# Performance work log

Hardware: AMD Instinct MI355X
Metric: run time of the kernel (lower is better)

The kernel has to match this reference:

```python
import jax, jax.numpy as jnp
import numpy as np

N_NODES = 50000


def _sage_conv(x, edge_index, W_l, W_r, b):
    """PyG SAGEConv (aggr='mean', root_weight=True):
    out[i] = mean_{j: (j->i) in E} x[j] @ W_l + x[i] @ W_r + b
    """
    src, dst = edge_index[0], edge_index[1]
    msgs = x[src]                                   # [E, d] gather
    agg = jax.ops.segment_sum(msgs, dst, num_segments=N_NODES)  # [N, d]
    deg = jax.ops.segment_sum(jnp.ones_like(dst, dtype=x.dtype), dst,
                              num_segments=N_NODES)
    agg = agg / jnp.maximum(deg, 1.0)[:, None]      # mean aggregation
    return agg @ W_l + x @ W_r + b


def setup_inputs() -> dict:
    key = jax.random.key(0)
    ks = jax.random.split(key, 8)
    d_in, d_hid, d_out = 128, 128, 64
    n_edges = 640000
    x = jax.random.normal(ks[0], (N_NODES, d_in), dtype=jnp.float32)
    edge_index = jax.random.randint(ks[1], (2, n_edges), 0, N_NODES, dtype=jnp.int32)
    s1 = 1.0 / np.sqrt(d_in)
    s2 = 1.0 / np.sqrt(d_hid)
    return {
        "x": x,
        "edge_index": edge_index,
        "W1_l": jax.random.uniform(ks[2], (d_in, d_hid), jnp.float32, -s1, s1),
        "W1_r": jax.random.uniform(ks[3], (d_in, d_hid), jnp.float32, -s1, s1),
        "b1": jnp.zeros((d_hid,), jnp.float32),
        "W2_l": jax.random.uniform(ks[4], (d_hid, d_out), jnp.float32, -s2, s2),
        "W2_r": jax.random.uniform(ks[5], (d_hid, d_out), jnp.float32, -s2, s2),
        "b2": jnp.zeros((d_out,), jnp.float32),
    }


def reference(x, edge_index, W1_l, W1_r, b1, W2_l, W2_r, b2):
    h = _sage_conv(x, edge_index, W1_l, W1_r, b1)
    h = jax.nn.relu(h)
    # Dropout(0.3) is identity in eval mode.
    return _sage_conv(h, edge_index, W2_l, W2_r, b2)
```

## Files before the change

kernel.cpp:

```cpp
#include <hip/hip_runtime.h>
#include <hip/hip_fp16.h>


typedef _Float16 half8 __attribute__((ext_vector_type(8)));
typedef float floatx4 __attribute__((ext_vector_type(4)));

#define NB 256
#define PA 320

__global__ __launch_bounds__(256) void prep_deg_kernel(const float* __restrict__ x,
                                                       const float* __restrict__ W1l, const float* __restrict__ W1r,
                                                       const float* __restrict__ W2l, const float* __restrict__ W2r,
                                                       _Float16* __restrict__ Ah,
                                                       _Float16* __restrict__ Bp1, _Float16* __restrict__ Bp2,
                                                       const int* __restrict__ dst, int* __restrict__ degi,
                                                       int N, int E) {
    int nconv = (N * 64 + 255) / 256;
    int b = blockIdx.x;
    int tid = threadIdx.x;
    if (b < nconv) {
        int i = b * 256 + tid;
        if (i < N * 64) {
            int row = i >> 6, c = i & 63;
            float2 v = ((const float2*)x)[(size_t)row * 64 + c];
            __half2 h2 = __floats2half2_rn(v.x, v.y);
            *(__half2*)(Ah + (size_t)row * 256 + 128 + c * 2) = h2;
        }
    } else if (b < nconv + 128) {
        int t = (b - nconv) * 256 + tid;
        int j = t & 7, lane = (t >> 3) & 63, nrep = (t >> 9) & 7, kt = t >> 12;
        int k = kt * 32 + ((lane >> 4) * 8) + j;
        int col = nrep * 16 + (lane & 15);
        float v = (k < 128) ? W1l[k * 128 + col] : W1r[(k - 128) * 128 + col];
        Bp1[t] = (_Float16)v;
    } else if (b < nconv + 192) {
        int t = (b - nconv - 128) * 256 + tid;
        int j = t & 7, lane = (t >> 3) & 63, nrep = (t >> 9) & 7, kt = t >> 12;
        int k = kt * 32 + ((lane >> 4) * 8) + j;
        int col = nrep * 16 + (lane & 15);
        float v = (col < 64) ? W2l[k * 64 + col] : W2r[k * 64 + (col - 64)];
        Bp2[t] = (_Float16)v;
    } else {
        int i = (b - nconv - 192) * 256 + tid;
        int E4 = E >> 2;
        if (i < E4) {
            int4 d = ((const int4*)dst)[i];
            atomicAdd(&degi[d.x], 1);
            atomicAdd(&degi[d.y], 1);
            atomicAdd(&degi[d.z], 1);
            atomicAdd(&degi[d.w], 1);
        }
        if (i == 0) {
            for (int e = E4 << 2; e < E; ++e) atomicAdd(&degi[dst[e]], 1);
        }
    }
}

__global__ __launch_bounds__(256) void scan_pass1(const int* __restrict__ deg, int* __restrict__ incl,
                                                  int* __restrict__ bsum, int N) {
    int tid = threadIdx.x;
    int i = blockIdx.x * 256 + tid;
    int v = (i < N) ? deg[i] : 0;
    int lane = tid & 63, wid = tid >> 6;
    int s = v;
#pragma unroll
    for (int off = 1; off < 64; off <<= 1) { int t = __shfl_up(s, off); if (lane >= off) s += t; }
    __shared__ int ws[4], wo[4];
    if (lane == 63) ws[wid] = s;
    __syncthreads();
    if (tid == 0) { int a = 0; for (int w = 0; w < 4; ++w) { wo[w] = a; a += ws[w]; } bsum[blockIdx.x] = a; }
    __syncthreads();
    s += wo[wid];
    if (i < N) incl[i] = s;
}

__global__ __launch_bounds__(256) void scan_pass3f(const int* __restrict__ incl, const int* __restrict__ bsum,
                                                   const int* __restrict__ degi,
                                                   int* __restrict__ rp, float* __restrict__ inv,
                                                   int* __restrict__ bcur, int N, int nper, int nblk) {
    __shared__ int sx[256];
    int tid = threadIdx.x;
    int v = (tid < nblk) ? bsum[tid] : 0;
    int lane = tid & 63, wid = tid >> 6;
    int s = v;
#pragma unroll
    for (int off = 1; off < 64; off <<= 1) { int t = __shfl_up(s, off); if (lane >= off) s += t; }
    __shared__ int ws[4], wo[4];
    if (lane == 63) ws[wid] = s;
    __syncthreads();
    if (tid == 0) { int a = 0; for (int w = 0; w < 4; ++w) { wo[w] = a; a += ws[w]; } }
    __syncthreads();
    sx[tid] = s + wo[wid] - v;
    __syncthreads();
    int boffv = sx[blockIdx.x];
    int i = blockIdx.x * 256 + tid;
    if (i < N) {
        int r = boffv + incl[i];
        rp[i + 1] = r;
        inv[i] = 1.0f / fmaxf((float)degi[i], 1.0f);
        if (i == 0) { rp[0] = 0; bcur[0] = 0; }
        int ip1 = i + 1;
        if (ip1 % nper == 0 && ip1 / nper < NB) bcur[ip1 / nper] = r;
    }
}

__global__ __launch_bounds__(256) void partA_kernel(const int* __restrict__ src, const int* __restrict__ dst,
                                                    int* __restrict__ bcur, unsigned int* __restrict__ bek,
                                                    int E, int nper) {
    __shared__ int cnt[NB], base[NB], cur[NB];
    int tid = threadIdx.x;
    int chunk = (E + PA - 1) / PA;
    int e0 = blockIdx.x * chunk;
    int e1 = min(e0 + chunk, E);
    cnt[tid] = 0;
    cur[tid] = 0;
    __syncthreads();
    for (int e = e0 + tid; e < e1; e += 256) {
        int d = dst[e];
        atomicAdd(&cnt[d / nper], 1);
    }
    __syncthreads();
    int c = cnt[tid];
    base[tid] = (c > 0) ? atomicAdd(&bcur[tid], c) : 0;
    __syncthreads();
    for (int e = e0 + tid; e < e1; e += 256) {
        int d = dst[e];
        int b = d / nper;
        int pos = base[b] + atomicAdd(&cur[b], 1);
        bek[pos] = ((unsigned int)src[e] << 8) | (unsigned int)(d - b * nper);
    }
}

__global__ __launch_bounds__(256) void partB_kernel(const unsigned int* __restrict__ bek,
                                                    const int* __restrict__ rp, int* __restrict__ csr,
                                                    int N, int nper) {
    __shared__ int rps[256], cur[256];
    int k = blockIdx.x;
    int lo = k * nper;
    int hi = min(lo + nper, N);
    int cntN = hi - lo;
    if (cntN <= 0) return;
    int tid = threadIdx.x;
    if (tid < cntN) { rps[tid] = rp[lo + tid]; cur[tid] = 0; }
    __syncthreads();
    int ebeg = rp[lo], eend = rp[hi];
    for (int j = ebeg + tid; j < eend; j += 256) {
        unsigned int u = bek[j];
        int loc = (int)(u & 0xffu);
        int s = (int)(u >> 8);
        int pos = rps[loc] + atomicAdd(&cur[loc], 1);
        csr[pos] = s;
    }
}

__global__ __launch_bounds__(256) void agg128h_kernel(const int* __restrict__ rp, const int* __restrict__ ci,
                                                      _Float16* __restrict__ Ah,
                                                      const float* __restrict__ inv, int N) {
    int node = (blockIdx.x * 256 + threadIdx.x) >> 6;
    int lane = threadIdx.x & 63;
    if (node >= N) return;
    int beg = rp[node], end = rp[node + 1];
    const uint* xu = (const uint*)Ah;
    float2 acc = make_float2(0.f, 0.f);
    for (int base = beg; base < end; base += 64) {
        int idx = base + lane;
        int sv = (idx < end) ? ci[idx] : 0;
        int cnt = min(64, end - base);
        int j = 0;
        for (; j + 8 <= cnt; j += 8) {
            uint u[8];
#pragma unroll
            for (int w = 0; w < 8; ++w) {
                int s = __shfl(sv, j + w);
                u[w] = xu[(size_t)s * 128 + 64 + lane];
            }
#pragma unroll
            for (int w = 0; w < 8; ++w) {
                float2 f = __half22float2(*(const __half2*)&u[w]);
                acc.x += f.x; acc.y += f.y;
            }
        }
        for (; j + 4 <= cnt; j += 4) {
            uint u[4];
#pragma unroll
            for (int w = 0; w < 4; ++w) {
                int s = __shfl(sv, j + w);
                u[w] = xu[(size_t)s * 128 + 64 + lane];
            }
#pragma unroll
            for (int w = 0; w < 4; ++w) {
                float2 f = __half22float2(*(const __half2*)&u[w]);
                acc.x += f.x; acc.y += f.y;
            }
        }
        for (; j < cnt; ++j) {
            int s = __shfl(sv, j);
            uint u = xu[(size_t)s * 128 + 64 + lane];
            float2 f = __half22float2(*(const __half2*)&u);
            acc.x += f.x; acc.y += f.y;
        }
    }
    float iv = inv[node];
    __half2 o = __floats2half2_rn(acc.x * iv, acc.y * iv);
    ((uint*)Ah)[(size_t)node * 128 + lane] = *(const uint*)&o;
}

__global__ __launch_bounds__(256) void agg64h_kernel(const int* __restrict__ rp, const int* __restrict__ ci,
                                                     const _Float16* __restrict__ hl,
                                                     const float* __restrict__ inv,
                                                     float* __restrict__ out, int N) {
    int node = (blockIdx.x * 256 + threadIdx.x) >> 5;
    int sl = threadIdx.x & 31;
    if (node >= N) return;
    int beg = rp[node], end = rp[node + 1];
    const uint* hu = (const uint*)hl;
    float2 acc = make_float2(0.f, 0.f);
    for (int base = beg; base < end; base += 32) {
        int idx = base + sl;
        int sv = (idx < end) ? ci[idx] : 0;
        int cnt = min(32, end - base);
        int j = 0;
        for (; j + 8 <= cnt; j += 8) {
            uint u[8];
#pragma unroll
            for (int w = 0; w < 8; ++w) {
                int s = __shfl(sv, j + w, 32);
                u[w] = hu[(size_t)s * 32 + sl];
            }
#pragma unroll
            for (int w = 0; w < 8; ++w) {
                float2 f = __half22float2(*(const __half2*)&u[w]);
                acc.x += f.x; acc.y += f.y;
            }
        }
        for (; j + 4 <= cnt; j += 4) {
            uint u[4];
#pragma unroll
            for (int w = 0; w < 4; ++w) {
                int s = __shfl(sv, j + w, 32);
                u[w] = hu[(size_t)s * 32 + sl];
            }
#pragma unroll
            for (int w = 0; w < 4; ++w) {
                float2 f = __half22float2(*(const __half2*)&u[w]);
                acc.x += f.x; acc.y += f.y;
            }
        }
        for (; j < cnt; ++j) {
            int s = __shfl(sv, j, 32);
            uint u = hu[(size_t)s * 32 + sl];
            float2 f = __half22float2(*(const __half2*)&u);
            acc.x += f.x; acc.y += f.y;
        }
    }
    float iv = inv[node];
    float2* op = (float2*)(out + (size_t)node * 64 + sl * 2);
    float2 cur = *op;
    cur.x += iv * acc.x;
    cur.y += iv * acc.y;
    *op = cur;
}

__global__ __launch_bounds__(256) void gemm1_mfma(const _Float16* __restrict__ Ah,
                                                  const _Float16* __restrict__ Bp,
                                                  const float* __restrict__ b1,
                                                  _Float16* __restrict__ hh, int N) {
    int wid = threadIdx.x >> 6, lane = threadIdx.x & 63;
    int r = lane & 15, q = lane >> 4;
    int rowbase = blockIdx.x * 128 + wid * 32;
    size_t ra = (size_t)min(rowbase + r, N - 1);
    size_t rb = (size_t)min(rowbase + 16 + r, N - 1);
    const half8* B8 = (const half8*)Bp;

    floatx4 acc[2][8];
#pragma unroll
    for (int m = 0; m < 2; ++m)
#pragma unroll
        for (int n = 0; n < 8; ++n) acc[m][n] = (floatx4){0.f, 0.f, 0.f, 0.f};

#pragma unroll
    for (int kt = 0; kt < 8; ++kt) {
        int k0 = kt * 32 + q * 8;
        half8 a0 = *(const half8*)(Ah + ra * 256 + k0);
        half8 a1 = *(const half8*)(Ah + rb * 256 + k0);
#pragma unroll
        for (int n = 0; n < 8; ++n) {
            half8 bf = B8[(kt * 8 + n) * 64 + lane];
            acc[0][n] = __builtin_amdgcn_mfma_f32_16x16x32_f16(a0, bf, acc[0][n], 0, 0, 0);
            acc[1][n] = __builtin_amdgcn_mfma_f32_16x16x32_f16(a1, bf, acc[1][n], 0, 0, 0);
        }
    }
    float bias[8];
#pragma unroll
    for (int n = 0; n < 8; ++n) bias[n] = b1[n * 16 + r];
#pragma unroll
    for (int m = 0; m < 2; ++m)
#pragma unroll
        for (int reg = 0; reg < 4; ++reg) {
            int row = rowbase + m * 16 + q * 4 + reg;
            if (row < N) {
                _Float16* p = hh + (size_t)row * 128 + r;
#pragma unroll
                for (int n = 0; n < 8; ++n)
                    p[n * 16] = (_Float16)fmaxf(acc[m][n][reg] + bias[n], 0.f);
            }
        }
}

__global__ __launch_bounds__(256) void gemm2_mfma(const _Float16* __restrict__ hh,
                                                  const _Float16* __restrict__ Bp,
                                                  const float* __restrict__ b2,
                                                  _Float16* __restrict__ hl,
                                                  float* __restrict__ outp, int N) {
    int wid = threadIdx.x >> 6, lane = threadIdx.x & 63;
    int r = lane & 15, q = lane >> 4;
    int rowbase = blockIdx.x * 128 + wid * 32;
    size_t ra = (size_t)min(rowbase + r, N - 1);
    size_t rb = (size_t)min(rowbase + 16 + r, N - 1);
    const half8* B8 = (const half8*)Bp;

    floatx4 acc[2][8];
#pragma unroll
    for (int m = 0; m < 2; ++m)
#pragma unroll
        for (int n = 0; n < 8; ++n) acc[m][n] = (floatx4){0.f, 0.f, 0.f, 0.f};

#pragma unroll
    for (int kt = 0; kt < 4; ++kt) {
        int k0 = kt * 32 + q * 8;
        half8 a0 = *(const half8*)(hh + ra * 128 + k0);
        half8 a1 = *(const half8*)(hh + rb * 128 + k0);
#pragma unroll
        for (int n = 0; n < 8; ++n) {
            half8 bf = B8[(kt * 8 + n) * 64 + lane];
            acc[0][n] = __builtin_amdgcn_mfma_f32_16x16x32_f16(a0, bf, acc[0][n], 0, 0, 0);
            acc[1][n] = __builtin_amdgcn_mfma_f32_16x16x32_f16(a1, bf, acc[1][n], 0, 0, 0);
        }
    }
    float bias[4];
#pragma unroll
    for (int n = 0; n < 4; ++n) bias[n] = b2[n * 16 + r];
#pragma unroll
    for (int m = 0; m < 2; ++m)
#pragma unroll
        for (int reg = 0; reg < 4; ++reg) {
            int row = rowbase + m * 16 + q * 4 + reg;
            if (row < N) {
                _Float16* ph = hl + (size_t)row * 64 + r;
                float* po = outp + (size_t)row * 64 + r;
#pragma unroll
                for (int n = 0; n < 4; ++n)
                    ph[n * 16] = (_Float16)acc[m][n][reg];
#pragma unroll
                for (int n = 0; n < 4; ++n)
                    po[n * 16] = acc[m][n + 4][reg] + bias[n];
            }
        }
}

extern "C" void kernel_launch(void* const* d_in, const int* in_sizes, int n_in,
                              void* d_out, int out_size, void* d_ws, size_t ws_size,
                              hipStream_t stream) {
    const float* x   = (const float*)d_in[0];
    const int*   ei  = (const int*)d_in[1];
    const float* W1l = (const float*)d_in[2];
    const float* W1r = (const float*)d_in[3];
    const float* b1  = (const float*)d_in[4];
    const float* W2l = (const float*)d_in[5];
    const float* W2r = (const float*)d_in[6];
    const float* b2  = (const float*)d_in[7];
    float* out = (float*)d_out;

    const int N = in_sizes[0] / 128;
    const int E = in_sizes[1] / 2;
    const int* srcv = ei;
    const int* dstv = ei + E;
    const int nper = (N + NB - 1) / NB;

    _Float16* Ah  = (_Float16*)d_ws;
    _Float16* hh  = Ah + (size_t)N * 256;
    _Float16* hl  = hh + (size_t)N * 128;
    _Float16* Bp1 = hl + (size_t)N * 64;
    _Float16* Bp2 = Bp1 + 32768;
    float* inv  = (float*)(Bp2 + 16384);
    int*   rp   = (int*)(inv + N);
    int*   degi = rp + (N + 1);
    int*   incl = degi + N;
    int*   csr  = incl + N;
    unsigned int* bek = (unsigned int*)(csr + E);
    int*   bsum = (int*)(bek + E);
    int*   bcur = bsum + 256;

    const int nsblk = (N + 255) / 256;

    hipMemsetAsync(degi, 0, (size_t)N * sizeof(int), stream);

    int nconv = (N * 64 + 255) / 256;
    int ndeg = ((E >> 2) + 255) / 256;
    prep_deg_kernel<<<nconv + 192 + ndeg, 256, 0, stream>>>(x, W1l, W1r, W2l, W2r,
                                                            Ah, Bp1, Bp2, dstv, degi, N, E);

    scan_pass1<<<nsblk, 256, 0, stream>>>(degi, incl, bsum, N);
    scan_pass3f<<<nsblk, 256, 0, stream>>>(incl, bsum, degi, rp, inv, bcur, N, nper, nsblk);

    partA_kernel<<<PA, 256, 0, stream>>>(srcv, dstv, bcur, bek, E, nper);
    partB_kernel<<<NB, 256, 0, stream>>>(bek, rp, csr, N, nper);

    agg128h_kernel<<<(N * 64 + 255) / 256, 256, 0, stream>>>(rp, csr, Ah, inv, N);
    int nb = (N + 127) / 128;
    gemm1_mfma<<<nb, 256, 0, stream>>>(Ah, Bp1, b1, hh, N);

    gemm2_mfma<<<nb, 256, 0, stream>>>(hh, Bp2, b2, hl, out, N);
    agg64h_kernel<<<(N * 32 + 255) / 256, 256, 0, stream>>>(rp, csr, hl, inv, out, N);
}
```

Baseline: 149.9 us.

## Replace per-node degree scan with bucket histogram and in-bucket local scan

Drops the global per-node degree atomics and the two-pass N-element scan. Prep now builds a 256-bucket histogram in shared memory, a single-block kernel scans it, and partB computes per-node counts, row pointers and inverse degrees locally within each bucket. This removes a memset of N ints, global atomic contention and two kernel launches, at the cost of an extra pass over bucketed edges in partB.

```diff
diff --git a/kernel.cpp b/kernel.cpp
--- a/kernel.cpp
+++ b/kernel.cpp
@@ -7,14 +7,16 @@
 
 #define NB 256
 #define PA 320
-
-__global__ __launch_bounds__(256) void prep_deg_kernel(const float* __restrict__ x,
-                                                       const float* __restrict__ W1l, const float* __restrict__ W1r,
-                                                       const float* __restrict__ W2l, const float* __restrict__ W2r,
-                                                       _Float16* __restrict__ Ah,
-                                                       _Float16* __restrict__ Bp1, _Float16* __restrict__ Bp2,
-                                                       const int* __restrict__ dst, int* __restrict__ degi,
-                                                       int N, int E) {
+#define HB 320
+
+__global__ __launch_bounds__(256) void prep_hist_kernel(const float* __restrict__ x,
+                                                        const float* __restrict__ W1l, const float* __restrict__ W1r,
+                                                        const float* __restrict__ W2l, const float* __restrict__ W2r,
+                                                        _Float16* __restrict__ Ah,
+                                                        _Float16* __restrict__ Bp1, _Float16* __restrict__ Bp2,
+                                                        const int* __restrict__ dst, int* __restrict__ ghist,
+                                                        int N, int E, int nper) {
+    __shared__ int lh[NB];
     int nconv = (N * 64 + 255) / 256;
     int b = blockIdx.x;
     int tid = threadIdx.x;
@@ -41,26 +43,22 @@
         float v = (col < 64) ? W2l[k * 64 + col] : W2r[k * 64 + (col - 64)];
         Bp2[t] = (_Float16)v;
     } else {
-        int i = (b - nconv - 192) * 256 + tid;
-        int E4 = E >> 2;
-        if (i < E4) {
-            int4 d = ((const int4*)dst)[i];
-            atomicAdd(&degi[d.x], 1);
-            atomicAdd(&degi[d.y], 1);
-            atomicAdd(&degi[d.z], 1);
-            atomicAdd(&degi[d.w], 1);
-        }
-        if (i == 0) {
-            for (int e = E4 << 2; e < E; ++e) atomicAdd(&degi[dst[e]], 1);
-        }
-    }
-}
-
-__global__ __launch_bounds__(256) void scan_pass1(const int* __restrict__ deg, int* __restrict__ incl,
-                                                  int* __restrict__ bsum, int N) {
+        int hb = b - nconv - 192;
+        lh[tid] = 0;
+        __syncthreads();
+        int chunk = (E + HB - 1) / HB;
+        int e0 = hb * chunk, e1 = min(e0 + chunk, E);
+        for (int e = e0 + tid; e < e1; e += 256) atomicAdd(&lh[dst[e] / nper], 1);
+        __syncthreads();
+        int c = lh[tid];
+        if (c) atomicAdd(&ghist[tid], c);
+    }
+}
+
+__global__ __launch_bounds__(256) void scan256_kernel(const int* __restrict__ ghist,
+                                                      int* __restrict__ bbase, int* __restrict__ bcur) {
     int tid = threadIdx.x;
-    int i = blockIdx.x * 256 + tid;
-    int v = (i < N) ? deg[i] : 0;
+    int v = ghist[tid];
     int lane = tid & 63, wid = tid >> 6;
     int s = v;
 #pragma unroll
@@ -68,40 +66,12 @@
     __shared__ int ws[4], wo[4];
     if (lane == 63) ws[wid] = s;
     __syncthreads();
-    if (tid == 0) { int a = 0; for (int w = 0; w < 4; ++w) { wo[w] = a; a += ws[w]; } bsum[blockIdx.x] = a; }
+    if (tid == 0) { int a = 0; for (int w = 0; w < 4; ++w) { wo[w] = a; a += ws[w]; } }
     __syncthreads();
     s += wo[wid];
-    if (i < N) incl[i] = s;
-}
-
-__global__ __launch_bounds__(256) void scan_pass3f(const int* __restrict__ incl, const int* __restrict__ bsum,
-                                                   const int* __restrict__ degi,
-                                                   int* __restrict__ rp, float* __restrict__ inv,
-                                                   int* __restrict__ bcur, int N, int nper, int nblk) {
-    __shared__ int sx[256];
-    int tid = threadIdx.x;
-    int v = (tid < nblk) ? bsum[tid] : 0;
-    int lane = tid & 63, wid = tid >> 6;
-    int s = v;
-#pragma unroll
-    for (int off = 1; off < 64; off <<= 1) { int t = __shfl_up(s, off); if (lane >= off) s += t; }
-    __shared__ int ws[4], wo[4];
-    if (lane == 63) ws[wid] = s;
-    __syncthreads();
-    if (tid == 0) { int a = 0; for (int w = 0; w < 4; ++w) { wo[w] = a; a += ws[w]; } }
-    __syncthreads();
-    sx[tid] = s + wo[wid] - v;
-    __syncthreads();
-    int boffv = sx[blockIdx.x];
-    int i = blockIdx.x * 256 + tid;
-    if (i < N) {
-        int r = boffv + incl[i];
-        rp[i + 1] = r;
-        inv[i] = 1.0f / fmaxf((float)degi[i], 1.0f);
-        if (i == 0) { rp[0] = 0; bcur[0] = 0; }
-        int ip1 = i + 1;
-        if (ip1 % nper == 0 && ip1 / nper < NB) bcur[ip1 / nper] = r;
-    }
+    bbase[tid] = s - v;
+    bcur[tid]  = s - v;
+    if (tid == 255) bbase[NB] = s;
 }
 
 __global__ __launch_bounds__(256) void partA_kernel(const int* __restrict__ src, const int* __restrict__ dst,
@@ -131,25 +101,45 @@
     }
 }
 
-__global__ __launch_bounds__(256) void partB_kernel(const unsigned int* __restrict__ bek,
-                                                    const int* __restrict__ rp, int* __restrict__ csr,
-                                                    int N, int nper) {
-    __shared__ int rps[256], cur[256];
+__global__ __launch_bounds__(256) void partB2_kernel(const unsigned int* __restrict__ bek,
+                                                     const int* __restrict__ bbase,
+                                                     int* __restrict__ rp, float* __restrict__ inv,
+                                                     int* __restrict__ csr, int N, int nper) {
+    __shared__ int lcnt[256], excl[256], cur[256];
+    __shared__ int ws[4], wo[4];
     int k = blockIdx.x;
     int lo = k * nper;
     int hi = min(lo + nper, N);
     int cntN = hi - lo;
     if (cntN <= 0) return;
     int tid = threadIdx.x;
-    if (tid < cntN) { rps[tid] = rp[lo + tid]; cur[tid] = 0; }
-    __syncthreads();
-    int ebeg = rp[lo], eend = rp[hi];
+    lcnt[tid] = 0; cur[tid] = 0;
+    __syncthreads();
+    int ebeg = bbase[k], eend = bbase[k + 1];
+    for (int j = ebeg + tid; j < eend; j += 256)
+        atomicAdd(&lcnt[bek[j] & 0xffu], 1);
+    __syncthreads();
+    int v = lcnt[tid];
+    int lane = tid & 63, wid = tid >> 6;
+    int s = v;
+#pragma unroll
+    for (int off = 1; off < 64; off <<= 1) { int t = __shfl_up(s, off); if (lane >= off) s += t; }
+    if (lane == 63) ws[wid] = s;
+    __syncthreads();
+    if (tid == 0) { int a = 0; for (int w = 0; w < 4; ++w) { wo[w] = a; a += ws[w]; } }
+    __syncthreads();
+    excl[tid] = s + wo[wid] - v;
+    __syncthreads();
+    if (tid <= cntN) {
+        int node = lo + tid;
+        if (node <= N) rp[node] = ebeg + excl[tid];
+        if (tid < cntN) inv[node] = 1.0f / fmaxf((float)lcnt[tid], 1.0f);
+    }
     for (int j = ebeg + tid; j < eend; j += 256) {
         unsigned int u = bek[j];
         int loc = (int)(u & 0xffu);
-        int s = (int)(u >> 8);
-        int pos = rps[loc] + atomicAdd(&cur[loc], 1);
-        csr[pos] = s;
+        int pos = ebeg + excl[loc] + atomicAdd(&cur[loc], 1);
+        csr[pos] = (int)(u >> 8);
     }
 }
 
@@ -384,27 +374,21 @@
     _Float16* Bp2 = Bp1 + 32768;
     float* inv  = (float*)(Bp2 + 16384);
     int*   rp   = (int*)(inv + N);
-    int*   degi = rp + (N + 1);
-    int*   incl = degi + N;
-    int*   csr  = incl + N;
+    int*   csr  = rp + (N + 1);
     unsigned int* bek = (unsigned int*)(csr + E);
-    int*   bsum = (int*)(bek + E);
-    int*   bcur = bsum + 256;
-
-    const int nsblk = (N + 255) / 256;
-
-    hipMemsetAsync(degi, 0, (size_t)N * sizeof(int), stream);
+    int*   ghist = (int*)(bek + E);
+    int*   bbase = ghist + NB;
+    int*   bcur  = bbase + (NB + 1);
+
+    hipMemsetAsync(ghist, 0, (size_t)NB * sizeof(int), stream);
 
     int nconv = (N * 64 + 255) / 256;
-    int ndeg = ((E >> 2) + 255) / 256;
-    prep_deg_kernel<<<nconv + 192 + ndeg, 256, 0, stream>>>(x, W1l, W1r, W2l, W2r,
-                                                            Ah, Bp1, Bp2, dstv, degi, N, E);
-
-    scan_pass1<<<nsblk, 256, 0, stream>>>(degi, incl, bsum, N);
-    scan_pass3f<<<nsblk, 256, 0, stream>>>(incl, bsum, degi, rp, inv, bcur, N, nper, nsblk);
-
+    prep_hist_kernel<<<nconv + 192 + HB, 256, 0, stream>>>(x, W1l, W1r, W2l, W2r,
+                                                           Ah, Bp1, Bp2, dstv, ghist, N, E, nper);
+
+    scan256_kernel<<<1, 256, 0, stream>>>(ghist, bbase, bcur);
     partA_kernel<<<PA, 256, 0, stream>>>(srcv, dstv, bcur, bek, E, nper);
-    partB_kernel<<<NB, 256, 0, stream>>>(bek, rp, csr, N, nper);
+    partB2_kernel<<<NB, 256, 0, stream>>>(bek, bbase, rp, inv, csr, N, nper);
 
     agg128h_kernel<<<(N * 64 + 255) / 256, 256, 0, stream>>>(rp, csr, Ah, inv, N);
     int nb = (N + 127) / 128;
```

After: 127.0 us. 15.3% less time.
